# Kernel optimization log

Hardware: AMD Instinct MI355X
Metric: run time of the kernel (lower is better)

Reference implementation:

```python
import jax, jax.numpy as jnp
import numpy as np

B, L, H = 32, 1024, 1024


def setup_inputs() -> dict:
    key = jax.random.key(0)
    ks = jax.random.split(key, 6)
    s = 1.0 / np.sqrt(H)
    return {
        "query": jax.random.normal(ks[0], (B, L, H), dtype=jnp.float32),
        "key": jax.random.normal(ks[1], (B, L, H), dtype=jnp.float32),
        "value": jax.random.normal(ks[2], (B, L, H), dtype=jnp.float32),
        "W": jax.random.normal(ks[3], (H, H), dtype=jnp.float32) * s,
        "mlp_w": jax.random.normal(ks[4], (1, 2 * H), dtype=jnp.float32) * s,
        "mlp_b": jnp.zeros((1,), dtype=jnp.float32),
    }


def reference(query, key, value, W, mlp_w, mlp_b):
    # Shared projection W (Linear, no bias): x @ W.T
    q = jnp.einsum("blh,oh->blo", query, W)
    k = jnp.einsum("blh,oh->blo", key, W)
    v = jnp.einsum("blh,oh->blo", value, W)
    # sim_mlp(cat([q,k],-1)) == q @ w1.T + k @ w2.T + b  (avoids materializing concat)
    w1, w2 = mlp_w[:, :H], mlp_w[:, H:]  # each [1, H]
    logits = jax.nn.relu(
        jnp.einsum("blh,oh->blo", q, w1) + jnp.einsum("blh,oh->blo", k, w2) + mlp_b
    )  # [B, L, 1]
    score = jax.nn.softmax(logits, axis=-2)  # softmax over L
    result = jnp.sum(score * v, axis=-2)  # [B, H]
    return result, score
```

## Files before the change

### kernel.cpp

```cpp
#include <hip/hip_runtime.h>

#define HDIM 1024
#define BDIM 32
#define LDIM 1024


__global__ __launch_bounds__(256) void k_u12(const float4* __restrict__ W4,
                                             const float* __restrict__ mlp_w,
                                             float* __restrict__ u1,
                                             float* __restrict__ u2) {
    int t  = threadIdx.x;
    int o0 = blockIdx.x * 16;
    float4 s1 = make_float4(0.f, 0.f, 0.f, 0.f);
    float4 s2 = make_float4(0.f, 0.f, 0.f, 0.f);
    #pragma unroll 4
    for (int o = o0; o < o0 + 16; ++o) {
        float4 w = W4[o * 256 + t];
        float c1 = mlp_w[o];
        float c2 = mlp_w[HDIM + o];
        s1.x += w.x * c1; s1.y += w.y * c1; s1.z += w.z * c1; s1.w += w.w * c1;
        s2.x += w.x * c2; s2.y += w.y * c2; s2.z += w.z * c2; s2.w += w.w * c2;
    }
    int h = t * 4;
    atomicAdd(&u1[h + 0], s1.x); atomicAdd(&u1[h + 1], s1.y);
    atomicAdd(&u1[h + 2], s1.z); atomicAdd(&u1[h + 3], s1.w);
    atomicAdd(&u2[h + 0], s2.x); atomicAdd(&u2[h + 1], s2.y);
    atomicAdd(&u2[h + 2], s2.z); atomicAdd(&u2[h + 3], s2.w);
}

__global__ __launch_bounds__(256, 4) void k_logits(const float4* __restrict__ q,
                                                   const float4* __restrict__ k,
                                                   const float4* __restrict__ u1v,
                                                   const float4* __restrict__ u2v,
                                                   const float* __restrict__ mlp_b,
                                                   float* __restrict__ logits) {
    int t = threadIdx.x;
    int lane = t & 63, wave = t >> 6;
    float4 a1[4], a2[4];
    #pragma unroll
    for (int i = 0; i < 4; ++i) {
        a1[i] = u1v[lane + 64 * i];
        a2[i] = u2v[lane + 64 * i];
    }
    float bias = mlp_b[0];
    long long wid = (long long)blockIdx.x * 4 + wave;
    #pragma unroll 2
    for (int r = 0; r < 4; ++r) {
        long long row = wid * 4 + r;
        const float4* qr = q + row * 256;
        const float4* kr = k + row * 256;
        float acc = 0.f;
        #pragma unroll
        for (int i = 0; i < 4; ++i) {
            float4 x = qr[lane + 64 * i];
            acc += x.x * a1[i].x + x.y * a1[i].y + x.z * a1[i].z + x.w * a1[i].w;
            float4 y = kr[lane + 64 * i];
            acc += y.x * a2[i].x + y.y * a2[i].y + y.z * a2[i].z + y.w * a2[i].w;
        }
        #pragma unroll
        for (int off = 32; off > 0; off >>= 1)
            acc += __shfl_down(acc, off, 64);
        if (lane == 0) {
            float v = acc + bias;
            logits[row] = v > 0.f ? v : 0.f;
        }
    }
}

__global__ __launch_bounds__(256) void k_softmax(const float* __restrict__ logits,
                                                 float* __restrict__ score) {
    __shared__ float sm[4];
    __shared__ float ss[4];
    int b = blockIdx.x;
    int t = threadIdx.x;
    int wave = t >> 6, lane = t & 63;
    float4 v = ((const float4*)(logits + b * LDIM))[t];
    float m = fmaxf(fmaxf(v.x, v.y), fmaxf(v.z, v.w));
    #pragma unroll
    for (int off = 32; off > 0; off >>= 1)
        m = fmaxf(m, __shfl_down(m, off, 64));
    if (lane == 0) sm[wave] = m;
    __syncthreads();
    float M = fmaxf(fmaxf(sm[0], sm[1]), fmaxf(sm[2], sm[3]));
    float4 e;
    e.x = __expf(v.x - M); e.y = __expf(v.y - M);
    e.z = __expf(v.z - M); e.w = __expf(v.w - M);
    float s = e.x + e.y + e.z + e.w;
    #pragma unroll
    for (int off = 32; off > 0; off >>= 1)
        s += __shfl_down(s, off, 64);
    if (lane == 0) ss[wave] = s;
    __syncthreads();
    float inv = 1.f / (ss[0] + ss[1] + ss[2] + ss[3]);
    float4 o;
    o.x = e.x * inv; o.y = e.y * inv; o.z = e.z * inv; o.w = e.w * inv;
    ((float4*)(score + b * LDIM))[t] = o;
}

__global__ __launch_bounds__(256, 4) void k_vbar(const float4* __restrict__ value,
                                                 const float* __restrict__ score,
                                                 float* __restrict__ vbar) {
    int b  = blockIdx.x >> 4;
    int lc = blockIdx.x & 15;
    int t  = threadIdx.x;
    const float4* vrow = value + ((long long)b * LDIM + lc * 64) * 256 + t;
    const float*  sc   = score + b * LDIM + lc * 64;
    float4 acc0 = make_float4(0.f, 0.f, 0.f, 0.f);
    float4 acc1 = make_float4(0.f, 0.f, 0.f, 0.f);
    #pragma unroll 4
    for (int l = 0; l < 64; l += 2) {
        float s0  = sc[l];
        float4 v0 = vrow[(long long)l * 256];
        acc0.x += s0 * v0.x; acc0.y += s0 * v0.y; acc0.z += s0 * v0.z; acc0.w += s0 * v0.w;
        float s1  = sc[l + 1];
        float4 v1 = vrow[(long long)(l + 1) * 256];
        acc1.x += s1 * v1.x; acc1.y += s1 * v1.y; acc1.z += s1 * v1.z; acc1.w += s1 * v1.w;
    }
    float* dst = vbar + b * HDIM + t * 4;
    atomicAdd(dst + 0, acc0.x + acc1.x);
    atomicAdd(dst + 1, acc0.y + acc1.y);
    atomicAdd(dst + 2, acc0.z + acc1.z);
    atomicAdd(dst + 3, acc0.w + acc1.w);
}

__global__ __launch_bounds__(256, 4) void k_result(const float4* __restrict__ W4,
                                                   const float4* __restrict__ vbar4,
                                                   float* __restrict__ result) {
    int t = threadIdx.x;
    int lane = t & 63, wave = t >> 6;
    int o = blockIdx.x * 4 + wave;
    float4 w[4];
    #pragma unroll
    for (int i = 0; i < 4; ++i)
        w[i] = W4[o * 256 + lane + 64 * i];
    for (int b = 0; b < BDIM; b += 2) {
        float acc0 = 0.f, acc1 = 0.f;
        #pragma unroll
        for (int i = 0; i < 4; ++i) {
            float4 v0 = vbar4[b * 256 + lane + 64 * i];
            acc0 += v0.x * w[i].x + v0.y * w[i].y + v0.z * w[i].z + v0.w * w[i].w;
            float4 v1 = vbar4[(b + 1) * 256 + lane + 64 * i];
            acc1 += v1.x * w[i].x + v1.y * w[i].y + v1.z * w[i].z + v1.w * w[i].w;
        }
        #pragma unroll
        for (int off = 32; off > 0; off >>= 1) {
            acc0 += __shfl_down(acc0, off, 64);
            acc1 += __shfl_down(acc1, off, 64);
        }
        if (lane == 0) {
            result[b * HDIM + o]       = acc0;
            result[(b + 1) * HDIM + o] = acc1;
        }
    }
}

extern "C" void kernel_launch(void* const* d_in, const int* in_sizes, int n_in,
                              void* d_out, int out_size, void* d_ws, size_t ws_size,
                              hipStream_t stream) {
    const float* query = (const float*)d_in[0];
    const float* key   = (const float*)d_in[1];
    const float* value = (const float*)d_in[2];
    const float* W     = (const float*)d_in[3];
    const float* mlp_w = (const float*)d_in[4];
    const float* mlp_b = (const float*)d_in[5];

    float* out    = (float*)d_out;
    float* result = out;
    float* score  = out + BDIM * LDIM;

    float* u1     = (float*)d_ws;
    float* u2     = u1 + HDIM;
    float* vbar   = u2 + HDIM;
    float* logits = vbar + BDIM * HDIM;

    hipMemsetAsync(d_ws, 0, (size_t)(2 * HDIM + BDIM * HDIM) * sizeof(float), stream);

    k_u12<<<64, 256, 0, stream>>>((const float4*)W, mlp_w, u1, u2);
    k_logits<<<2048, 256, 0, stream>>>((const float4*)query, (const float4*)key,
                                       (const float4*)u1, (const float4*)u2, mlp_b, logits);
    k_softmax<<<BDIM, 256, 0, stream>>>(logits, score);
    k_vbar<<<BDIM * 16, 256, 0, stream>>>((const float4*)value, score, vbar);
    k_result<<<256, 256, 0, stream>>>((const float4*)W, (const float4*)vbar, out);
}
```

Before: 380.2 us.

## Repartition logits, vbar and result kernels for more parallelism and block reductions

The logits kernel now has each block process 8 rows, with all 256 threads covering a full row and a cross-wave shared-memory reduction. This replaces the earlier scheme of one wave per row looping over 4 rows. The vbar kernel splits work over H chunks and L slices across 2048 blocks, with the waves in a block interleaving over L and reducing through shared memory before the atomic add. The result kernel splits the batch across twice as many blocks. The goal is higher occupancy and more memory-level parallelism on these bandwidth-bound streams, at the cost of extra block syncs and smaller per-block work.

```diff
diff --git a/kernel.cpp b/kernel.cpp
--- a/kernel.cpp
+++ b/kernel.cpp
@@ -4,6 +4,10 @@
 #define BDIM 32
 #define LDIM 1024
 
+
+__device__ __forceinline__ float dot4(float4 a, float4 b) {
+    return a.x * b.x + a.y * b.y + a.z * b.z + a.w * b.w;
+}
 
 __global__ __launch_bounds__(256) void k_u12(const float4* __restrict__ W4,
                                              const float* __restrict__ mlp_w,
@@ -28,42 +32,45 @@
     atomicAdd(&u2[h + 2], s2.z); atomicAdd(&u2[h + 3], s2.w);
 }
 
-__global__ __launch_bounds__(256, 4) void k_logits(const float4* __restrict__ q,
+__global__ __launch_bounds__(256, 8) void k_logits(const float4* __restrict__ q,
                                                    const float4* __restrict__ k,
                                                    const float4* __restrict__ u1v,
                                                    const float4* __restrict__ u2v,
                                                    const float* __restrict__ mlp_b,
                                                    float* __restrict__ logits) {
+    __shared__ float sm[8][4];
     int t = threadIdx.x;
     int lane = t & 63, wave = t >> 6;
-    float4 a1[4], a2[4];
-    #pragma unroll
-    for (int i = 0; i < 4; ++i) {
-        a1[i] = u1v[lane + 64 * i];
-        a2[i] = u2v[lane + 64 * i];
-    }
-    float bias = mlp_b[0];
-    long long wid = (long long)blockIdx.x * 4 + wave;
-    #pragma unroll 2
-    for (int r = 0; r < 4; ++r) {
-        long long row = wid * 4 + r;
-        const float4* qr = q + row * 256;
-        const float4* kr = k + row * 256;
-        float acc = 0.f;
-        #pragma unroll
-        for (int i = 0; i < 4; ++i) {
-            float4 x = qr[lane + 64 * i];
-            acc += x.x * a1[i].x + x.y * a1[i].y + x.z * a1[i].z + x.w * a1[i].w;
-            float4 y = kr[lane + 64 * i];
-            acc += y.x * a2[i].x + y.y * a2[i].y + y.z * a2[i].z + y.w * a2[i].w;
-        }
-        #pragma unroll
-        for (int off = 32; off > 0; off >>= 1)
-            acc += __shfl_down(acc, off, 64);
-        if (lane == 0) {
-            float v = acc + bias;
-            logits[row] = v > 0.f ? v : 0.f;
-        }
+    float4 a1 = u1v[t];
+    float4 a2 = u2v[t];
+    long long r0 = (long long)blockIdx.x * 8;
+    const float4* qb = q + r0 * 256 + t;
+    const float4* kb = k + r0 * 256 + t;
+
+    float p[8];
+    #pragma unroll
+    for (int r = 0; r < 8; r += 2) {
+        float4 xq0 = qb[(r + 0) * 256];
+        float4 xk0 = kb[(r + 0) * 256];
+        float4 xq1 = qb[(r + 1) * 256];
+        float4 xk1 = kb[(r + 1) * 256];
+        p[r + 0] = dot4(xq0, a1) + dot4(xk0, a2);
+        p[r + 1] = dot4(xq1, a1) + dot4(xk1, a2);
+    }
+    #pragma unroll
+    for (int off = 32; off > 0; off >>= 1)
+        #pragma unroll
+        for (int r = 0; r < 8; ++r)
+            p[r] += __shfl_down(p[r], off, 64);
+    if (lane == 0) {
+        #pragma unroll
+        for (int r = 0; r < 8; ++r)
+            sm[r][wave] = p[r];
+    }
+    __syncthreads();
+    if (t < 8) {
+        float v = sm[t][0] + sm[t][1] + sm[t][2] + sm[t][3] + mlp_b[0];
+        logits[r0 + t] = v > 0.f ? v : 0.f;
     }
 }
 
@@ -97,30 +104,48 @@
     ((float4*)(score + b * LDIM))[t] = o;
 }
 
-__global__ __launch_bounds__(256, 4) void k_vbar(const float4* __restrict__ value,
+__global__ __launch_bounds__(256, 8) void k_vbar(const float4* __restrict__ value,
                                                  const float* __restrict__ score,
                                                  float* __restrict__ vbar) {
-    int b  = blockIdx.x >> 4;
-    int lc = blockIdx.x & 15;
-    int t  = threadIdx.x;
-    const float4* vrow = value + ((long long)b * LDIM + lc * 64) * 256 + t;
-    const float*  sc   = score + b * LDIM + lc * 64;
-    float4 acc0 = make_float4(0.f, 0.f, 0.f, 0.f);
-    float4 acc1 = make_float4(0.f, 0.f, 0.f, 0.f);
-    #pragma unroll 4
-    for (int l = 0; l < 64; l += 2) {
-        float s0  = sc[l];
-        float4 v0 = vrow[(long long)l * 256];
-        acc0.x += s0 * v0.x; acc0.y += s0 * v0.y; acc0.z += s0 * v0.z; acc0.w += s0 * v0.w;
-        float s1  = sc[l + 1];
-        float4 v1 = vrow[(long long)(l + 1) * 256];
-        acc1.x += s1 * v1.x; acc1.y += s1 * v1.y; acc1.z += s1 * v1.z; acc1.w += s1 * v1.w;
-    }
-    float* dst = vbar + b * HDIM + t * 4;
-    atomicAdd(dst + 0, acc0.x + acc1.x);
-    atomicAdd(dst + 1, acc0.y + acc1.y);
-    atomicAdd(dst + 2, acc0.z + acc1.z);
-    atomicAdd(dst + 3, acc0.w + acc1.w);
+    __shared__ float4 red[3][64];
+    int bid = blockIdx.x;
+    int b  = bid >> 6;
+    int hc = (bid >> 4) & 3;
+    int ls = bid & 15;
+    int t = threadIdx.x, lane = t & 63, wave = t >> 6;
+    const float4* vb = value + ((long long)(b * LDIM + ls * 64) * 256) + hc * 64 + lane;
+    const float*  sc = score + b * LDIM + ls * 64;
+    float4 acc = make_float4(0.f, 0.f, 0.f, 0.f);
+    #pragma unroll 1
+    for (int j = 0; j < 16; j += 4) {
+        int l0 = wave + 4 * (j + 0);
+        int l1 = wave + 4 * (j + 1);
+        int l2 = wave + 4 * (j + 2);
+        int l3 = wave + 4 * (j + 3);
+        float4 v0 = vb[l0 * 256];
+        float4 v1 = vb[l1 * 256];
+        float4 v2 = vb[l2 * 256];
+        float4 v3 = vb[l3 * 256];
+        float s0 = sc[l0], s1 = sc[l1], s2 = sc[l2], s3 = sc[l3];
+        acc.x += s0 * v0.x + s1 * v1.x + s2 * v2.x + s3 * v3.x;
+        acc.y += s0 * v0.y + s1 * v1.y + s2 * v2.y + s3 * v3.y;
+        acc.z += s0 * v0.z + s1 * v1.z + s2 * v2.z + s3 * v3.z;
+        acc.w += s0 * v0.w + s1 * v1.w + s2 * v2.w + s3 * v3.w;
+    }
+    if (wave > 0) red[wave - 1][lane] = acc;
+    __syncthreads();
+    if (wave == 0) {
+        float4 r0 = red[0][lane], r1 = red[1][lane], r2 = red[2][lane];
+        acc.x += r0.x + r1.x + r2.x;
+        acc.y += r0.y + r1.y + r2.y;
+        acc.z += r0.z + r1.z + r2.z;
+        acc.w += r0.w + r1.w + r2.w;
+        float* dst = vbar + b * HDIM + hc * 256 + lane * 4;
+        atomicAdd(dst + 0, acc.x);
+        atomicAdd(dst + 1, acc.y);
+        atomicAdd(dst + 2, acc.z);
+        atomicAdd(dst + 3, acc.w);
+    }
 }
 
 __global__ __launch_bounds__(256, 4) void k_result(const float4* __restrict__ W4,
@@ -128,12 +153,13 @@
                                                    float* __restrict__ result) {
     int t = threadIdx.x;
     int lane = t & 63, wave = t >> 6;
-    int o = blockIdx.x * 4 + wave;
+    int o  = (blockIdx.x & 255) * 4 + wave;
+    int b0 = (blockIdx.x >> 8) * 16;
     float4 w[4];
     #pragma unroll
     for (int i = 0; i < 4; ++i)
         w[i] = W4[o * 256 + lane + 64 * i];
-    for (int b = 0; b < BDIM; b += 2) {
+    for (int b = b0; b < b0 + 16; b += 2) {
         float acc0 = 0.f, acc1 = 0.f;
         #pragma unroll
         for (int i = 0; i < 4; ++i) {
@@ -176,9 +202,9 @@
     hipMemsetAsync(d_ws, 0, (size_t)(2 * HDIM + BDIM * HDIM) * sizeof(float), stream);
 
     k_u12<<<64, 256, 0, stream>>>((const float4*)W, mlp_w, u1, u2);
-    k_logits<<<2048, 256, 0, stream>>>((const float4*)query, (const float4*)key,
+    k_logits<<<4096, 256, 0, stream>>>((const float4*)query, (const float4*)key,
                                        (const float4*)u1, (const float4*)u2, mlp_b, logits);
     k_softmax<<<BDIM, 256, 0, stream>>>(logits, score);
-    k_vbar<<<BDIM * 16, 256, 0, stream>>>((const float4*)value, score, vbar);
-    k_result<<<256, 256, 0, stream>>>((const float4*)W, (const float4*)vbar, out);
-}
+    k_vbar<<<2048, 256, 0, stream>>>((const float4*)value, score, vbar);
+    k_result<<<512, 256, 0, stream>>>((const float4*)W, (const float4*)vbar, out);
+}
```

Result: no change. 375.3 us (-1.3%).
